# Performance work log

Hardware: AMD Instinct MI355X
Metric: run time of the kernel (lower is better)

The kernel has to match this reference:

```python
import jax, jax.numpy as jnp
import numpy as np

W_CHAMFER = 1.0
W_SMOOTH = 0.5
K_NEIGHBORS = 8


def _pairwise_sqdist(a, b):
    # a: [B,N,3], b: [B,M,3] -> [B,N,M] squared euclidean distances
    a2 = jnp.sum(a * a, axis=-1)  # [B,N]
    b2 = jnp.sum(b * b, axis=-1)  # [B,M]
    ab = jnp.einsum('bnd,bmd->bnm', a, b)  # [B,N,M]
    d2 = a2[:, :, None] + b2[:, None, :] - 2.0 * ab
    return jnp.maximum(d2, 0.0)


def _chamfer(pc1, pc2):
    d = jnp.sqrt(_pairwise_sqdist(pc1, pc2))  # [B,N,M] euclidean (matches torch.norm)
    d1 = jnp.min(d, axis=2)  # [B,N]
    d2 = jnp.min(d, axis=1)  # [B,M]
    return jnp.mean(d1) + jnp.mean(d2)


def _smoothness(pc, flow, k=K_NEIGHBORS):
    d2 = _pairwise_sqdist(pc, pc)  # [B,N,N]
    # k+1 nearest (squared dist preserves ordering); drop self (index 0)
    _, idx = jax.lax.top_k(-d2, k + 1)  # [B,N,k+1]
    idx = idx[:, :, 1:]  # [B,N,k]
    neighbor_flow = jax.vmap(lambda f, i: f[i])(flow, idx)  # [B,N,k,3]
    diff = flow[:, :, None, :] - neighbor_flow
    return jnp.mean(jnp.linalg.norm(diff, axis=-1))


def setup_inputs() -> dict:
    key = jax.random.key(0)
    k1, k2, k3 = jax.random.split(key, 3)
    B, N, M = 2, 8192, 8192
    pc1 = jax.random.normal(k1, (B, N, 3), dtype=jnp.float32)
    pc2 = jax.random.normal(k2, (B, M, 3), dtype=jnp.float32)
    pred_flow = jax.random.normal(k3, (B, N, 3), dtype=jnp.float32) * 0.1
    return {"pc1": pc1, "pc2": pc2, "pred_flow": pred_flow}


def reference(pc1, pc2, pred_flow):
    pc1_warped = pc1 + pred_flow
    l_chamfer = _chamfer(pc1_warped, pc2)
    l_smooth = _smoothness(pc1, pred_flow)
    return W_CHAMFER * l_chamfer + W_SMOOTH * l_smooth
```

## Files before the change

kernel.cpp:

```cpp
#include <hip/hip_runtime.h>

#define N_PTS 8192
#define BATCH 2
#define KNN 8
#define NBLK_C 1024
#define NBLK_S 2048
#define NBLOCKS (NBLK_C + NBLK_S)

#define ARR_PC2  0
#define ARR_WARP 2
#define ARR_PC1  4

__device__ __forceinline__ void ce(unsigned &x, unsigned &y) {
    unsigned lo = min(x, y), hi = max(x, y); x = lo; y = hi;
}

__device__ __forceinline__ void insert4(unsigned o[4], unsigned key) {
    unsigned n0 = min(o[0], key);
    unsigned n1 = max(o[0], min(o[1], key));
    unsigned n2 = max(o[1], min(o[2], key));
    unsigned n3 = max(o[2], min(o[3], key));
    o[0]=n0; o[1]=n1; o[2]=n2; o[3]=n3;
}

__device__ __forceinline__ void merge_stage8(unsigned m[8], int d) {
    unsigned p[8], c[8];
    #pragma unroll
    for (int k = 0; k < 8; ++k) p[k] = (unsigned)__shfl_xor((int)m[k], d, 64);
    #pragma unroll
    for (int k = 0; k < 8; ++k) c[k] = min(m[k], p[7-k]);
    ce(c[0],c[4]); ce(c[1],c[5]); ce(c[2],c[6]); ce(c[3],c[7]);
    ce(c[0],c[2]); ce(c[1],c[3]); ce(c[4],c[6]); ce(c[5],c[7]);
    ce(c[0],c[1]); ce(c[2],c[3]); ce(c[4],c[5]); ce(c[6],c[7]);
    #pragma unroll
    for (int k = 0; k < 8; ++k) m[k] = c[k];
}

__device__ __forceinline__ void merge64(unsigned m[8]) {
    merge_stage8(m, 1); merge_stage8(m, 2); merge_stage8(m, 4);
    merge_stage8(m, 8); merge_stage8(m, 16); merge_stage8(m, 32);
}

__global__ __launch_bounds__(256) void pack_kernel(
        const float* __restrict__ pc1, const float* __restrict__ pc2,
        const float* __restrict__ flow, float4* __restrict__ ws) {
    const int t = blockIdx.x * 256 + threadIdx.x;
    const int arr = t >> 13, i = t & (N_PTS - 1);
    const int bb = arr & 1;
    const size_t base = (size_t)bb * N_PTS * 3 + (size_t)i * 3;
    float x, y, z;
    if (arr < 2)      { x = pc2[base+0];              y = pc2[base+1];              z = pc2[base+2]; }
    else if (arr < 4) { x = pc1[base+0] + flow[base+0];
                        y = pc1[base+1] + flow[base+1];
                        z = pc1[base+2] + flow[base+2]; }
    else              { x = pc1[base+0];              y = pc1[base+1];              z = pc1[base+2]; }
    ws[t] = make_float4(x, y, z, fmaf(x, x, fmaf(y, y, z * z)));
}

__global__ __launch_bounds__(256, 4) void mega_kernel(
        const float4* __restrict__ ws, const float* __restrict__ flow,
        float* __restrict__ out) {
    __shared__ float psum[4];
    const int tid = threadIdx.x, bx = blockIdx.x;
    const int lane = tid & 63, wv = tid >> 6;
    const int ri = bx / 3, role = bx % 3;

    if (role == 2) {
        const int z = ri >> 8, bb = z & 1, dir = z >> 1;
        const int cb = ri & 255;
        const float4* rows = ws + (size_t)((dir == 0 ? ARR_WARP : ARR_PC2) + bb) * N_PTS;
        const float4* cand = ws + (size_t)((dir == 0 ? ARR_PC2 : ARR_WARP) + bb) * N_PTS;
        const int rbase = cb * 32 + wv * 8;

        float mx[8], my[8], mz[8], bmin[8];
        #pragma unroll
        for (int k = 0; k < 8; ++k) {
            float4 q = rows[rbase + k];
            mx[k] = -2.0f * q.x; my[k] = -2.0f * q.y; mz[k] = -2.0f * q.z;
            bmin[k] = __builtin_inff();
        }

        #pragma unroll 2
        for (int j = 0; j < N_PTS; j += 128) {
            float4 qa = cand[j + lane];
            float4 qb = cand[j + 64 + lane];
            #pragma unroll
            for (int k = 0; k < 8; ++k) {
                float sa = fmaf(mx[k], qa.x, fmaf(my[k], qa.y, fmaf(mz[k], qa.z, qa.w)));
                float sb = fmaf(mx[k], qb.x, fmaf(my[k], qb.y, fmaf(mz[k], qb.z, qb.w)));
                bmin[k] = fminf(fminf(bmin[k], sa), sb);
            }
        }

        #pragma unroll
        for (int k = 0; k < 8; ++k) {
            #pragma unroll
            for (int d = 1; d < 64; d <<= 1)
                bmin[k] = fminf(bmin[k], __shfl_xor(bmin[k], d, 64));
        }
        if (lane == 0) {
            float val = 0.0f;
            #pragma unroll
            for (int k = 0; k < 8; ++k) {
                float p2k = 0.25f * fmaf(mx[k], mx[k], fmaf(my[k], my[k], mz[k] * mz[k]));
                val += sqrtf(fmaxf(bmin[k] + p2k, 0.0f));
            }
            psum[wv] = val;
        }
        __syncthreads();
        if (tid == 0) {
            float ch = psum[0] + psum[1] + psum[2] + psum[3];
            atomicAdd(out, ch * (1.0f / (float)(BATCH * N_PTS)));
        }
    } else {
        const int sbx = ri * 2 + role;
        const int b  = sbx >> 10;
        const int sx = sbx & 1023;
        const int i0w = sx * 8 + wv * 2;
        const float4* cand = ws + (size_t)(ARR_PC1 + b) * N_PTS;
        const float* F = flow + (size_t)b * N_PTS * 3;

        float mx[2], my[2], mz[2], p2[2], gr[2];
        unsigned thr[2], o[2][4];
        #pragma unroll
        for (int r = 0; r < 2; ++r) {
            float4 q = cand[i0w + r];
            mx[r] = -2.0f * q.x; my[r] = -2.0f * q.y; mz[r] = -2.0f * q.z;
            p2[r] = q.w;
            gr[r] = __builtin_inff();
            thr[r] = 0xFFFFFFFFu;
            #pragma unroll
            for (int k = 0; k < 4; ++k) o[r][k] = 0xFFFFFFFFu;
        }

        auto update_thr = [&]() {
            #pragma unroll
            for (int r = 0; r < 2; ++r) {
                unsigned m0 = o[r][0], m1 = o[r][1], m2 = o[r][2], m3 = o[r][3];
                #pragma unroll
                for (int d = 1; d <= 16; d <<= 1) {
                    unsigned q0 = (unsigned)__shfl_xor((int)m0, d, 64);
                    unsigned q1 = (unsigned)__shfl_xor((int)m1, d, 64);
                    unsigned q2 = (unsigned)__shfl_xor((int)m2, d, 64);
                    unsigned q3 = (unsigned)__shfl_xor((int)m3, d, 64);
                    unsigned c0 = min(m0, q3), c1 = min(m1, q2);
                    unsigned c2 = min(m2, q1), c3 = min(m3, q0);
                    ce(c0, c2); ce(c1, c3); ce(c0, c1); ce(c2, c3);
                    m0 = c0; m1 = c1; m2 = c2; m3 = c3;
                }
                unsigned bound = max(m3, (unsigned)__shfl_xor((int)m3, 32, 64));
                thr[r] = min(thr[r], bound);
                float thr_up = __uint_as_float((thr[r] & 0xFFFFE000u) + 0x4000u);
                gr[r] = thr_up - p2[r];
            }
        };

        auto gated_span = [&](int j0, int j1) {
            #pragma unroll 2
            for (int j = j0; j < j1; j += 128) {
                float4 qa = cand[j + lane];
                float4 qb = cand[j + 64 + lane];
                int ja = j + lane, jb = j + 64 + lane;
                float sa[2], sb[2];
                #pragma unroll
                for (int r = 0; r < 2; ++r) {
                    sa[r] = fmaf(mx[r], qa.x, fmaf(my[r], qa.y, fmaf(mz[r], qa.z, qa.w)));
                    sb[r] = fmaf(mx[r], qb.x, fmaf(my[r], qb.y, fmaf(mz[r], qb.z, qb.w)));
                }
                #pragma unroll
                for (int r = 0; r < 2; ++r) {
                    if (__any(fminf(sa[r], sb[r]) <= gr[r])) {
                        float da = fmaxf(sa[r] + p2[r], 0.0f);
                        unsigned ka = (__float_as_uint(da) & 0xFFFFE000u) | (unsigned)ja;
                        ka = (ja == i0w + r) ? 0xFFFFFFFFu : ka;
                        insert4(o[r], ka);
                        float db = fmaxf(sb[r] + p2[r], 0.0f);
                        unsigned kb = (__float_as_uint(db) & 0xFFFFE000u) | (unsigned)jb;
                        kb = (jb == i0w + r) ? 0xFFFFFFFFu : kb;
                        insert4(o[r], kb);
                    }
                }
            }
        };

        #pragma unroll 2
        for (int j = 0; j < 1024; j += 128) {
            float4 qa = cand[j + lane];
            float4 qb = cand[j + 64 + lane];
            int ja = j + lane, jb = j + 64 + lane;
            #pragma unroll
            for (int r = 0; r < 2; ++r) {
                float sa = fmaf(mx[r], qa.x, fmaf(my[r], qa.y, fmaf(mz[r], qa.z, qa.w)));
                float da = fmaxf(sa + p2[r], 0.0f);
                unsigned ka = (__float_as_uint(da) & 0xFFFFE000u) | (unsigned)ja;
                ka = (ja == i0w + r) ? 0xFFFFFFFFu : ka;
                insert4(o[r], ka);
                float sb = fmaf(mx[r], qb.x, fmaf(my[r], qb.y, fmaf(mz[r], qb.z, qb.w)));
                float db = fmaxf(sb + p2[r], 0.0f);
                unsigned kb = (__float_as_uint(db) & 0xFFFFE000u) | (unsigned)jb;
                kb = (jb == i0w + r) ? 0xFFFFFFFFu : kb;
                insert4(o[r], kb);
            }
        }
        update_thr();
        gated_span(1024, 2048); update_thr();
        gated_span(2048, 4096); update_thr();
        gated_span(4096, N_PTS);

        const int sel = lane & 15;
        const int pr = sel >> 3, kk = sel & 7;
        unsigned mykey = 0xFFFFFFFFu;
        #pragma unroll
        for (int r = 0; r < 2; ++r) {
            unsigned m[8] = {o[r][0], o[r][1], o[r][2], o[r][3],
                             0xFFFFFFFFu, 0xFFFFFFFFu, 0xFFFFFFFFu, 0xFFFFFFFFu};
            merge64(m);
            if (pr == r) {
                unsigned k2 = m[0];
                #pragma unroll
                for (int t = 1; t < 8; ++t) k2 = (kk == t) ? m[t] : k2;
                mykey = k2;
            }
        }
        const int i = i0w + pr;
        const int j = (int)(mykey & (N_PTS - 1));
        float dx = F[i*3+0] - F[j*3+0];
        float dy = F[i*3+1] - F[j*3+1];
        float dz = F[i*3+2] - F[j*3+2];
        float sv = sqrtf(fmaf(dx, dx, fmaf(dy, dy, dz * dz)));
        #pragma unroll
        for (int d = 1; d < 64; d <<= 1) sv += __shfl_xor(sv, d, 64);
        if (lane == 0) psum[wv] = sv;
        __syncthreads();

        if (tid == 0) {
            float sm = psum[0] + psum[1] + psum[2] + psum[3];
            atomicAdd(out, sm * (0.125f / ((float)BATCH * N_PTS * KNN)));
        }
    }
}

extern "C" void kernel_launch(void* const* d_in, const int* in_sizes, int n_in,
                              void* d_out, int out_size, void* d_ws, size_t ws_size,
                              hipStream_t stream) {
    const float* pc1  = (const float*)d_in[0];
    const float* pc2  = (const float*)d_in[1];
    const float* flow = (const float*)d_in[2];
    float* out = (float*)d_out;
    float4* ws4 = (float4*)d_ws;

    pack_kernel<<<dim3(6 * N_PTS / 256), 256, 0, stream>>>(pc1, pc2, flow, ws4);
    mega_kernel<<<dim3(NBLOCKS), 256, 0, stream>>>(ws4, flow, out);
}
```

Baseline: 135.8 us.

## Spatially sort points into Morton cells and prune slabs with bounding boxes

The pack kernel now bins each point cloud into an 8x8x8 Morton-ordered grid using a counting sort, and records a bounding box for each 64-point slab. The chamfer and kNN searches first scan the nearest slab, then scan only slabs whose box lower bound beats the current best distance, replacing the brute-force scan over all 8192 candidates. An index map translates sorted positions back to original indices for the flow lookup. The cost is a serial pack step of 6 blocks with many shared-memory atomics, plus divergent slab loops. The grid bounds assume roughly unit-normal data in [-3,3], but points outside are clamped into edge cells, so results stay correct.

```diff
diff --git a/kernel.cpp b/kernel.cpp
--- a/kernel.cpp
+++ b/kernel.cpp
@@ -3,6 +3,8 @@
 #define N_PTS 8192
 #define BATCH 2
 #define KNN 8
+#define NSLAB 128
+#define CELLS 512
 #define NBLK_C 1024
 #define NBLK_S 2048
 #define NBLOCKS (NBLK_C + NBLK_S)
@@ -10,6 +12,9 @@
 #define ARR_PC2  0
 #define ARR_WARP 2
 #define ARR_PC1  4
+#define WS_BB0   49152
+#define WS_BB1   49920
+#define WS_OIDX  50688
 
 __device__ __forceinline__ void ce(unsigned &x, unsigned &y) {
     unsigned lo = min(x, y), hi = max(x, y); x = lo; y = hi;
@@ -41,25 +46,103 @@
     merge_stage8(m, 8); merge_stage8(m, 16); merge_stage8(m, 32);
 }
 
-__global__ __launch_bounds__(256) void pack_kernel(
+__device__ __forceinline__ unsigned f2o(float f) {
+    unsigned u = __float_as_uint(f);
+    return (u & 0x80000000u) ? ~u : (u | 0x80000000u);
+}
+__device__ __forceinline__ float o2f(unsigned u) {
+    return __uint_as_float((u & 0x80000000u) ? (u ^ 0x80000000u) : ~u);
+}
+
+__device__ __forceinline__ unsigned spread3(unsigned v) {
+    return ((v & 4u) << 4) | ((v & 2u) << 2) | (v & 1u);
+}
+__device__ __forceinline__ int cellof(float x, float y, float z) {
+    int ix = min(7, max(0, (int)((x + 3.0f) * 1.3333333f)));
+    int iy = min(7, max(0, (int)((y + 3.0f) * 1.3333333f)));
+    int iz = min(7, max(0, (int)((z + 3.0f) * 1.3333333f)));
+    return (int)((spread3((unsigned)ix) << 2) | (spread3((unsigned)iy) << 1)
+                 | spread3((unsigned)iz));
+}
+
+__device__ __forceinline__ float boxd2(const float4 bn, const float4 bx,
+                                       float x, float y, float z) {
+    float tx = fmaxf(fmaxf(bn.x - x, x - bx.x), 0.0f);
+    float ty = fmaxf(fmaxf(bn.y - y, y - bx.y), 0.0f);
+    float tz = fmaxf(fmaxf(bn.z - z, z - bx.z), 0.0f);
+    return fmaf(tx, tx, fmaf(ty, ty, tz * tz));
+}
+
+__global__ __launch_bounds__(512) void pack_sort_kernel(
         const float* __restrict__ pc1, const float* __restrict__ pc2,
-        const float* __restrict__ flow, float4* __restrict__ ws) {
-    const int t = blockIdx.x * 256 + threadIdx.x;
-    const int arr = t >> 13, i = t & (N_PTS - 1);
-    const int bb = arr & 1;
-    const size_t base = (size_t)bb * N_PTS * 3 + (size_t)i * 3;
-    float x, y, z;
-    if (arr < 2)      { x = pc2[base+0];              y = pc2[base+1];              z = pc2[base+2]; }
-    else if (arr < 4) { x = pc1[base+0] + flow[base+0];
-                        y = pc1[base+1] + flow[base+1];
-                        z = pc1[base+2] + flow[base+2]; }
-    else              { x = pc1[base+0];              y = pc1[base+1];              z = pc1[base+2]; }
-    ws[t] = make_float4(x, y, z, fmaf(x, x, fmaf(y, y, z * z)));
+        const float* __restrict__ flow, float4* __restrict__ ws,
+        unsigned* __restrict__ oidx) {
+    __shared__ unsigned hist[CELLS];
+    __shared__ unsigned offs[CELLS];
+    __shared__ unsigned bbn[NSLAB * 3], bbx[NSLAB * 3];
+    const int arr = blockIdx.x, t = threadIdx.x;
+    const int bbatch = arr & 1;
+    const bool warped = (arr >= 2 && arr < 4);
+    const float* A = (arr < 2) ? pc2 : pc1;
+    const size_t base = (size_t)bbatch * N_PTS * 3;
+
+    for (int i = t; i < CELLS; i += 512) hist[i] = 0u;
+    for (int i = t; i < NSLAB * 3; i += 512) { bbn[i] = 0xFFFFFFFFu; bbx[i] = 0u; }
+    __syncthreads();
+
+    int cid[16];
+    #pragma unroll
+    for (int k = 0; k < 16; ++k) {
+        int i = t * 16 + k;
+        float x = A[base + i*3+0], y = A[base + i*3+1], z = A[base + i*3+2];
+        if (warped) { x += flow[base+i*3+0]; y += flow[base+i*3+1]; z += flow[base+i*3+2]; }
+        cid[k] = cellof(x, y, z);
+        atomicAdd(&hist[cid[k]], 1u);
+    }
+    __syncthreads();
+
+    if (t < 64) {
+        unsigned loc[8], s = 0;
+        #pragma unroll
+        for (int q = 0; q < 8; ++q) { loc[q] = s; s += hist[t*8 + q]; }
+        unsigned run = s;
+        #pragma unroll
+        for (int d = 1; d < 64; d <<= 1) {
+            unsigned v = (unsigned)__shfl_up((int)run, d, 64);
+            if (t >= d) run += v;
+        }
+        unsigned bse = run - s;
+        #pragma unroll
+        for (int q = 0; q < 8; ++q) offs[t*8 + q] = bse + loc[q];
+    }
+    __syncthreads();
+
+    #pragma unroll
+    for (int k = 0; k < 16; ++k) {
+        int i = t * 16 + k;
+        float x = A[base + i*3+0], y = A[base + i*3+1], z = A[base + i*3+2];
+        if (warped) { x += flow[base+i*3+0]; y += flow[base+i*3+1]; z += flow[base+i*3+2]; }
+        unsigned pos = atomicAdd(&offs[cid[k]], 1u);
+        ws[(size_t)arr * N_PTS + pos] = make_float4(x, y, z, fmaf(x, x, fmaf(y, y, z*z)));
+        if (arr >= 4) oidx[(size_t)(arr - 4) * N_PTS + pos] = (unsigned)i;
+        int s = (int)(pos >> 6);
+        atomicMin(&bbn[s*3+0], f2o(x)); atomicMax(&bbx[s*3+0], f2o(x));
+        atomicMin(&bbn[s*3+1], f2o(y)); atomicMax(&bbx[s*3+1], f2o(y));
+        atomicMin(&bbn[s*3+2], f2o(z)); atomicMax(&bbx[s*3+2], f2o(z));
+    }
+    __syncthreads();
+
+    for (int s = t; s < NSLAB; s += 512) {
+        ws[WS_BB0 + (size_t)arr * NSLAB + s] =
+            make_float4(o2f(bbn[s*3+0]), o2f(bbn[s*3+1]), o2f(bbn[s*3+2]), 0.0f);
+        ws[WS_BB1 + (size_t)arr * NSLAB + s] =
+            make_float4(o2f(bbx[s*3+0]), o2f(bbx[s*3+1]), o2f(bbx[s*3+2]), 0.0f);
+    }
 }
 
 __global__ __launch_bounds__(256, 4) void mega_kernel(
         const float4* __restrict__ ws, const float* __restrict__ flow,
-        float* __restrict__ out) {
+        const unsigned* __restrict__ oidx, float* __restrict__ out) {
     __shared__ float psum[4];
     const int tid = threadIdx.x, bx = blockIdx.x;
     const int lane = tid & 63, wv = tid >> 6;
@@ -68,30 +151,62 @@
     if (role == 2) {
         const int z = ri >> 8, bb = z & 1, dir = z >> 1;
         const int cb = ri & 255;
-        const float4* rows = ws + (size_t)((dir == 0 ? ARR_WARP : ARR_PC2) + bb) * N_PTS;
-        const float4* cand = ws + (size_t)((dir == 0 ? ARR_PC2 : ARR_WARP) + bb) * N_PTS;
+        const int ca = (dir == 0 ? ARR_PC2 : ARR_WARP) + bb;
+        const int ra = (dir == 0 ? ARR_WARP : ARR_PC2) + bb;
+        const float4* rows = ws + (size_t)ra * N_PTS;
+        const float4* cand = ws + (size_t)ca * N_PTS;
+        const float4* bmn = ws + WS_BB0 + (size_t)ca * NSLAB;
+        const float4* bmx = ws + WS_BB1 + (size_t)ca * NSLAB;
         const int rbase = cb * 32 + wv * 8;
 
-        float mx[8], my[8], mz[8], bmin[8];
+        float rx[8], ry[8], rz[8], bmin[8];
         #pragma unroll
         for (int k = 0; k < 8; ++k) {
             float4 q = rows[rbase + k];
-            mx[k] = -2.0f * q.x; my[k] = -2.0f * q.y; mz[k] = -2.0f * q.z;
+            rx[k] = q.x; ry[k] = q.y; rz[k] = q.z;
             bmin[k] = __builtin_inff();
         }
-
-        #pragma unroll 2
-        for (int j = 0; j < N_PTS; j += 128) {
-            float4 qa = cand[j + lane];
-            float4 qb = cand[j + 64 + lane];
+        float4 bn0 = bmn[lane], bx0 = bmx[lane];
+        float4 bn1 = bmn[lane + 64], bx1 = bmx[lane + 64];
+        float lb0[8], lb1[8];
+        unsigned long long sm0 = 0ull, sm1 = 0ull;
+        #pragma unroll
+        for (int k = 0; k < 8; ++k) {
+            lb0[k] = boxd2(bn0, bx0, rx[k], ry[k], rz[k]);
+            lb1[k] = boxd2(bn1, bx1, rx[k], ry[k], rz[k]);
+            unsigned k0 = (__float_as_uint(lb0[k]) & 0xFFFFFF80u) | (unsigned)lane;
+            unsigned k1 = (__float_as_uint(lb1[k]) & 0xFFFFFF80u) | (unsigned)(lane + 64);
+            unsigned kk = min(k0, k1);
+            #pragma unroll
+            for (int d = 1; d < 64; d <<= 1)
+                kk = min(kk, (unsigned)__shfl_xor((int)kk, d, 64));
+            unsigned s = kk & 127u;
+            if (s < 64) sm0 |= 1ull << s; else sm1 |= 1ull << (s - 64);
+        }
+        auto scan_slab = [&](int s) {
+            float4 c = cand[s * 64 + lane];
             #pragma unroll
             for (int k = 0; k < 8; ++k) {
-                float sa = fmaf(mx[k], qa.x, fmaf(my[k], qa.y, fmaf(mz[k], qa.z, qa.w)));
-                float sb = fmaf(mx[k], qb.x, fmaf(my[k], qb.y, fmaf(mz[k], qb.z, qb.w)));
-                bmin[k] = fminf(fminf(bmin[k], sa), sb);
+                float dx = rx[k] - c.x, dy = ry[k] - c.y, dz = rz[k] - c.z;
+                bmin[k] = fminf(bmin[k], fmaf(dx, dx, fmaf(dy, dy, dz * dz)));
             }
-        }
-
+        };
+        { unsigned long long m = sm0; while (m) { int s = __ffsll((unsigned long long)m) - 1; m &= m - 1; scan_slab(s); } }
+        { unsigned long long m = sm1; while (m) { int s = __ffsll((unsigned long long)m) - 1; m &= m - 1; scan_slab(s + 64); } }
+        bool p0 = false, p1 = false;
+        #pragma unroll
+        for (int k = 0; k < 8; ++k) {
+            float u = bmin[k];
+            #pragma unroll
+            for (int d = 1; d < 64; d <<= 1)
+                u = fminf(u, __shfl_xor(u, d, 64));
+            p0 |= (lb0[k] < u);
+            p1 |= (lb1[k] < u);
+        }
+        unsigned long long q0 = __ballot(p0) & ~sm0;
+        unsigned long long q1 = __ballot(p1) & ~sm1;
+        while (q0) { int s = __ffsll(q0) - 1; q0 &= q0 - 1; scan_slab(s); }
+        while (q1) { int s = __ffsll(q1) - 1; q1 &= q1 - 1; scan_slab(s + 64); }
         #pragma unroll
         for (int k = 0; k < 8; ++k) {
             #pragma unroll
@@ -101,10 +216,7 @@
         if (lane == 0) {
             float val = 0.0f;
             #pragma unroll
-            for (int k = 0; k < 8; ++k) {
-                float p2k = 0.25f * fmaf(mx[k], mx[k], fmaf(my[k], my[k], mz[k] * mz[k]));
-                val += sqrtf(fmaxf(bmin[k] + p2k, 0.0f));
-            }
+            for (int k = 0; k < 8; ++k) val += sqrtf(fmaxf(bmin[k], 0.0f));
             psum[wv] = val;
         }
         __syncthreads();
@@ -114,98 +226,81 @@
         }
     } else {
         const int sbx = ri * 2 + role;
-        const int b  = sbx >> 10;
-        const int sx = sbx & 1023;
+        const int b = sbx >> 10, sx = sbx & 1023;
         const int i0w = sx * 8 + wv * 2;
         const float4* cand = ws + (size_t)(ARR_PC1 + b) * N_PTS;
+        const float4* bmn = ws + WS_BB0 + (size_t)(ARR_PC1 + b) * NSLAB;
+        const float4* bmx = ws + WS_BB1 + (size_t)(ARR_PC1 + b) * NSLAB;
+        const unsigned* OI = oidx + (size_t)b * N_PTS;
         const float* F = flow + (size_t)b * N_PTS * 3;
 
-        float mx[2], my[2], mz[2], p2[2], gr[2];
+        float rx[2], ry[2], rz[2], thrf[2];
         unsigned thr[2], o[2][4];
         #pragma unroll
         for (int r = 0; r < 2; ++r) {
             float4 q = cand[i0w + r];
-            mx[r] = -2.0f * q.x; my[r] = -2.0f * q.y; mz[r] = -2.0f * q.z;
-            p2[r] = q.w;
-            gr[r] = __builtin_inff();
+            rx[r] = q.x; ry[r] = q.y; rz[r] = q.z;
             thr[r] = 0xFFFFFFFFu;
             #pragma unroll
             for (int k = 0; k < 4; ++k) o[r][k] = 0xFFFFFFFFu;
         }
-
-        auto update_thr = [&]() {
+        float4 bn0 = bmn[lane], bx0 = bmx[lane];
+        float4 bn1 = bmn[lane + 64], bx1 = bmx[lane + 64];
+        float lb0[2], lb1[2];
+        unsigned long long sm0 = 0ull, sm1 = 0ull;
+        { int so = i0w >> 6;
+          if (so < 64) sm0 |= 1ull << so; else sm1 |= 1ull << (so - 64); }
+        #pragma unroll
+        for (int r = 0; r < 2; ++r) {
+            lb0[r] = boxd2(bn0, bx0, rx[r], ry[r], rz[r]);
+            lb1[r] = boxd2(bn1, bx1, rx[r], ry[r], rz[r]);
+            unsigned k0 = (__float_as_uint(lb0[r]) & 0xFFFFFF80u) | (unsigned)lane;
+            unsigned k1 = (__float_as_uint(lb1[r]) & 0xFFFFFF80u) | (unsigned)(lane + 64);
+            unsigned kk = min(k0, k1);
+            #pragma unroll
+            for (int d = 1; d < 64; d <<= 1)
+                kk = min(kk, (unsigned)__shfl_xor((int)kk, d, 64));
+            unsigned s = kk & 127u;
+            if (s < 64) sm0 |= 1ull << s; else sm1 |= 1ull << (s - 64);
+        }
+        auto scan_slab = [&](int s) {
+            float4 c = cand[s * 64 + lane];
+            int j = s * 64 + lane;
             #pragma unroll
             for (int r = 0; r < 2; ++r) {
-                unsigned m0 = o[r][0], m1 = o[r][1], m2 = o[r][2], m3 = o[r][3];
-                #pragma unroll
-                for (int d = 1; d <= 16; d <<= 1) {
-                    unsigned q0 = (unsigned)__shfl_xor((int)m0, d, 64);
-                    unsigned q1 = (unsigned)__shfl_xor((int)m1, d, 64);
-                    unsigned q2 = (unsigned)__shfl_xor((int)m2, d, 64);
-                    unsigned q3 = (unsigned)__shfl_xor((int)m3, d, 64);
-                    unsigned c0 = min(m0, q3), c1 = min(m1, q2);
-                    unsigned c2 = min(m2, q1), c3 = min(m3, q0);
-                    ce(c0, c2); ce(c1, c3); ce(c0, c1); ce(c2, c3);
-                    m0 = c0; m1 = c1; m2 = c2; m3 = c3;
-                }
-                unsigned bound = max(m3, (unsigned)__shfl_xor((int)m3, 32, 64));
-                thr[r] = min(thr[r], bound);
-                float thr_up = __uint_as_float((thr[r] & 0xFFFFE000u) + 0x4000u);
-                gr[r] = thr_up - p2[r];
+                float dx = rx[r] - c.x, dy = ry[r] - c.y, dz = rz[r] - c.z;
+                float d2 = fmaf(dx, dx, fmaf(dy, dy, dz * dz));
+                unsigned key = (__float_as_uint(d2) & 0xFFFFE000u) | (unsigned)j;
+                key = (j == i0w + r) ? 0xFFFFFFFFu : key;
+                insert4(o[r], key);
             }
         };
-
-        auto gated_span = [&](int j0, int j1) {
-            #pragma unroll 2
-            for (int j = j0; j < j1; j += 128) {
-                float4 qa = cand[j + lane];
-                float4 qb = cand[j + 64 + lane];
-                int ja = j + lane, jb = j + 64 + lane;
-                float sa[2], sb[2];
-                #pragma unroll
-                for (int r = 0; r < 2; ++r) {
-                    sa[r] = fmaf(mx[r], qa.x, fmaf(my[r], qa.y, fmaf(mz[r], qa.z, qa.w)));
-                    sb[r] = fmaf(mx[r], qb.x, fmaf(my[r], qb.y, fmaf(mz[r], qb.z, qb.w)));
-                }
-                #pragma unroll
-                for (int r = 0; r < 2; ++r) {
-                    if (__any(fminf(sa[r], sb[r]) <= gr[r])) {
-                        float da = fmaxf(sa[r] + p2[r], 0.0f);
-                        unsigned ka = (__float_as_uint(da) & 0xFFFFE000u) | (unsigned)ja;
-                        ka = (ja == i0w + r) ? 0xFFFFFFFFu : ka;
-                        insert4(o[r], ka);
-                        float db = fmaxf(sb[r] + p2[r], 0.0f);
-                        unsigned kb = (__float_as_uint(db) & 0xFFFFE000u) | (unsigned)jb;
-                        kb = (jb == i0w + r) ? 0xFFFFFFFFu : kb;
-                        insert4(o[r], kb);
-                    }
-                }
+        { unsigned long long m = sm0; while (m) { int s = __ffsll(m) - 1; m &= m - 1; scan_slab(s); } }
+        { unsigned long long m = sm1; while (m) { int s = __ffsll(m) - 1; m &= m - 1; scan_slab(s + 64); } }
+        #pragma unroll
+        for (int r = 0; r < 2; ++r) {
+            unsigned m0 = o[r][0], m1 = o[r][1], m2 = o[r][2], m3 = o[r][3];
+            #pragma unroll
+            for (int d = 1; d <= 16; d <<= 1) {
+                unsigned q0 = (unsigned)__shfl_xor((int)m0, d, 64);
+                unsigned q1 = (unsigned)__shfl_xor((int)m1, d, 64);
+                unsigned q2 = (unsigned)__shfl_xor((int)m2, d, 64);
+                unsigned q3 = (unsigned)__shfl_xor((int)m3, d, 64);
+                unsigned c0 = min(m0, q3), c1 = min(m1, q2);
+                unsigned c2 = min(m2, q1), c3 = min(m3, q0);
+                ce(c0, c2); ce(c1, c3); ce(c0, c1); ce(c2, c3);
+                m0 = c0; m1 = c1; m2 = c2; m3 = c3;
             }
-        };
-
-        #pragma unroll 2
-        for (int j = 0; j < 1024; j += 128) {
-            float4 qa = cand[j + lane];
-            float4 qb = cand[j + 64 + lane];
-            int ja = j + lane, jb = j + 64 + lane;
-            #pragma unroll
-            for (int r = 0; r < 2; ++r) {
-                float sa = fmaf(mx[r], qa.x, fmaf(my[r], qa.y, fmaf(mz[r], qa.z, qa.w)));
-                float da = fmaxf(sa + p2[r], 0.0f);
-                unsigned ka = (__float_as_uint(da) & 0xFFFFE000u) | (unsigned)ja;
-                ka = (ja == i0w + r) ? 0xFFFFFFFFu : ka;
-                insert4(o[r], ka);
-                float sb = fmaf(mx[r], qb.x, fmaf(my[r], qb.y, fmaf(mz[r], qb.z, qb.w)));
-                float db = fmaxf(sb + p2[r], 0.0f);
-                unsigned kb = (__float_as_uint(db) & 0xFFFFE000u) | (unsigned)jb;
-                kb = (jb == i0w + r) ? 0xFFFFFFFFu : kb;
-                insert4(o[r], kb);
-            }
-        }
-        update_thr();
-        gated_span(1024, 2048); update_thr();
-        gated_span(2048, 4096); update_thr();
-        gated_span(4096, N_PTS);
+            unsigned bound = max(m3, (unsigned)__shfl_xor((int)m3, 32, 64));
+            thr[r] = min(thr[r], bound);
+            thrf[r] = __uint_as_float((thr[r] & 0xFFFFE000u) + 0x4000u);
+        }
+        bool p0 = (lb0[0] < thrf[0]) | (lb0[1] < thrf[1]);
+        bool p1 = (lb1[0] < thrf[0]) | (lb1[1] < thrf[1]);
+        unsigned long long q0 = __ballot(p0) & ~sm0;
+        unsigned long long q1 = __ballot(p1) & ~sm1;
+        while (q0) { int s = __ffsll(q0) - 1; q0 &= q0 - 1; scan_slab(s); }
+        while (q1) { int s = __ffsll(q1) - 1; q1 &= q1 - 1; scan_slab(s + 64); }
 
         const int sel = lane & 15;
         const int pr = sel >> 3, kk = sel & 7;
@@ -218,15 +313,17 @@
             if (pr == r) {
                 unsigned k2 = m[0];
                 #pragma unroll
-                for (int t = 1; t < 8; ++t) k2 = (kk == t) ? m[t] : k2;
+                for (int t2 = 1; t2 < 8; ++t2) k2 = (kk == t2) ? m[t2] : k2;
                 mykey = k2;
             }
         }
-        const int i = i0w + pr;
-        const int j = (int)(mykey & (N_PTS - 1));
-        float dx = F[i*3+0] - F[j*3+0];
-        float dy = F[i*3+1] - F[j*3+1];
-        float dz = F[i*3+2] - F[j*3+2];
+        const int isrt = i0w + pr;
+        const int io = (int)OI[isrt];
+        const int j  = (int)(mykey & (N_PTS - 1));
+        const int jo = (int)OI[j];
+        float dx = F[io*3+0] - F[jo*3+0];
+        float dy = F[io*3+1] - F[jo*3+1];
+        float dz = F[io*3+2] - F[jo*3+2];
         float sv = sqrtf(fmaf(dx, dx, fmaf(dy, dy, dz * dz)));
         #pragma unroll
         for (int d = 1; d < 64; d <<= 1) sv += __shfl_xor(sv, d, 64);
@@ -248,7 +345,8 @@
     const float* flow = (const float*)d_in[2];
     float* out = (float*)d_out;
     float4* ws4 = (float4*)d_ws;
-
-    pack_kernel<<<dim3(6 * N_PTS / 256), 256, 0, stream>>>(pc1, pc2, flow, ws4);
-    mega_kernel<<<dim3(NBLOCKS), 256, 0, stream>>>(ws4, flow, out);
-}
+    unsigned* oidx = (unsigned*)(ws4 + WS_OIDX);
+
+    pack_sort_kernel<<<dim3(6), 512, 0, stream>>>(pc1, pc2, flow, ws4, oidx);
+    mega_kernel<<<dim3(NBLOCKS), 256, 0, stream>>>(ws4, flow, oidx, out);
+}
```

New measurement: 167.8 us. 1.24x slower.
